# Performance work log

Measured on AMD Instinct MI355X. Metric: run time of the kernel, lower is better.

Reference implementation:

```python
import jax, jax.numpy as jnp
import numpy as np

CLIP_LIMIT = 40.0
TILES = 8  # tileGridSize=(8,8)
BINS = 256


def masked_normalize(x, mask, lo, hi):
    # Faithful to Preprocessor.normalize: if mask nonempty and masked max>0,
    # rescale masked values from [vmin,vmax] -> [lo,hi]; else set masked to lo.
    vmax = jnp.max(jnp.where(mask, x, -jnp.inf))
    vmin = jnp.min(jnp.where(mask, x, jnp.inf))
    cond = jnp.any(mask) & (vmax > 0.0)
    rng = jnp.maximum(vmax - vmin, jnp.float32(1e-12))  # guard degenerate case
    scaled = (x - vmin) / rng * (hi - lo) + lo
    return jnp.where(mask, jnp.where(cond, scaled, jnp.float32(lo)), x)


def clahe_apply(img, clip_limit, T):
    # img: (H, W) int32 in [0, 255]. OpenCV-style CLAHE: per-tile clipped
    # histogram equalization LUTs + bilinear interpolation between tile LUTs.
    H, W = img.shape
    th, tw = H // T, W // T
    area = th * tw
    # per-tile histograms via segment_sum (memory-light, no one-hot blowup)
    ty = jnp.arange(H, dtype=jnp.int32) // th
    tx = jnp.arange(W, dtype=jnp.int32) // tw
    tile_id = ty[:, None] * T + tx[None, :]  # (H, W)
    seg = (tile_id * BINS + img).reshape(-1)
    hist = jax.ops.segment_sum(
        jnp.ones(H * W, jnp.float32), seg, num_segments=T * T * BINS
    ).reshape(T * T, BINS)
    # clip + redistribute excess (uniform batch + stepped residual, OpenCV-style)
    cl = max(int(clip_limit * area / BINS), 1)
    excess = jnp.sum(jnp.maximum(hist - cl, 0.0), axis=1, keepdims=True)
    hist = jnp.minimum(hist, float(cl))
    batch = jnp.floor(excess / BINS)
    residual = excess - batch * BINS  # in [0, 256)
    ar = jnp.arange(BINS, dtype=jnp.float32)
    step = jnp.maximum(jnp.floor(BINS / jnp.maximum(residual, 1.0)), 1.0)
    res_add = ((jnp.mod(ar, step) == 0.0) & (jnp.floor(ar / step) < residual)).astype(jnp.float32)
    hist = hist + batch + res_add
    # LUT from CDF
    cdf = jnp.cumsum(hist, axis=1)
    lut = jnp.clip(jnp.round(cdf * (255.0 / area)), 0.0, 255.0).reshape(T, T, BINS)
    # bilinear interpolation between the 4 surrounding tile LUTs
    fy = (jnp.arange(H, dtype=jnp.float32) + 0.5) / th - 0.5
    fx = (jnp.arange(W, dtype=jnp.float32) + 0.5) / tw - 0.5
    y0 = jnp.clip(jnp.floor(fy).astype(jnp.int32), 0, T - 1)
    x0 = jnp.clip(jnp.floor(fx).astype(jnp.int32), 0, T - 1)
    y1 = jnp.clip(y0 + 1, 0, T - 1)
    x1 = jnp.clip(x0 + 1, 0, T - 1)
    wy = (fy - jnp.floor(fy))[:, None]  # (H,1); at clamped borders both LUTs equal
    wx = (fx - jnp.floor(fx))[None, :]  # (1,W)
    v00 = lut[y0[:, None], x0[None, :], img]
    v01 = lut[y0[:, None], x1[None, :], img]
    v10 = lut[y1[:, None], x0[None, :], img]
    v11 = lut[y1[:, None], x1[None, :], img]
    return (v00 * (1 - wy) * (1 - wx) + v01 * (1 - wy) * wx
            + v10 * wy * (1 - wx) + v11 * wy * wx)


def contrast(x):
    # (X*255).to(uint8) truncates; values in [0,1] so plain floor + clip
    xb = jnp.clip(jnp.floor(x * 255.0), 0.0, 255.0).astype(jnp.int32)
    zero = xb == 0
    nz_cnt = jnp.sum(~zero)
    mean_nz = jnp.floor(
        jnp.sum(jnp.where(zero, 0, xb).astype(jnp.float32)) / jnp.maximum(nz_cnt, 1)
    ).astype(jnp.int32)
    filled = jnp.where(zero & (nz_cnt > 0), mean_nz, xb)
    eq = clahe_apply(filled, CLIP_LIMIT, TILES)
    eq = jnp.where(zero, 0.0, eq)
    return eq / 255.0


def _process_channel(x):  # x: (H, W)
    mask = x > 0.0
    x = masked_normalize(x, mask, 0.0, 1.0)
    x = contrast(x)
    x = masked_normalize(x, mask, 1.0 / 255.0, 1.0)
    return x


def setup_inputs() -> dict:
    key = jax.random.key(0)
    X = jax.random.uniform(key, (1, 4, 4096, 4096), dtype=jnp.float32)
    return {"X": X}


def reference(X):
    # X: (1, C, H, W); channels are processed independently
    out = jax.vmap(_process_channel)(X[0])
    return out[None]
```

## Files before the change

### kernel.cpp

```cpp
#include <hip/hip_runtime.h>
#include <stdint.h>
#include <math.h>

#define NPC 16777216
#define NF4 4194304

struct ChScalars {
  int vmin1, vmax1;
  int vmin2, vmax2;
  int mean_nz, nzpos;
  int pad0, pad1;
};

__device__ __forceinline__ int binof(float x, int cond1, float vmin, float rng) {
  float t = (x > 0.0f) ? (cond1 ? (x - vmin) / rng : 0.0f) : x;
  float b = floorf(t * 255.0f);
  b = fminf(fmaxf(b, 0.0f), 255.0f);
  return (int)b;
}

__global__ __launch_bounds__(256) void k_init(ChScalars* S, unsigned* hist) {
  int g = blockIdx.x * 256 + threadIdx.x;
  hist[g] = 0u;
  if (g < 4) {
    S[g].vmin1 = 0x7FFFFFFF;
    S[g].vmax1 = 0;
    S[g].vmin2 = 0x7FFFFFFF;
    S[g].vmax2 = 0x80000000;
    S[g].mean_nz = 0;
    S[g].nzpos = 0;
    S[g].pad0 = 0; S[g].pad1 = 0;
  }
}

__global__ __launch_bounds__(256) void k_minmax1(const float* __restrict__ X,
                                                 ChScalars* __restrict__ S) {
  const int ch = blockIdx.y;
  const float4* xp = reinterpret_cast<const float4*>(X) + (size_t)ch * NF4;
  const int g = blockIdx.x * 256 + threadIdx.x;
  int mn = 0x7FFFFFFF, mx = 0;
  #pragma unroll
  for (int i = 0; i < 16; ++i) {
    float4 v = xp[(size_t)i * 262144 + g];
    if (v.x > 0.0f) { int b = __float_as_int(v.x); mn = min(mn, b); mx = max(mx, b); }
    if (v.y > 0.0f) { int b = __float_as_int(v.y); mn = min(mn, b); mx = max(mx, b); }
    if (v.z > 0.0f) { int b = __float_as_int(v.z); mn = min(mn, b); mx = max(mx, b); }
    if (v.w > 0.0f) { int b = __float_as_int(v.w); mn = min(mn, b); mx = max(mx, b); }
  }
  __shared__ int smn[256], smx[256];
  smn[threadIdx.x] = mn; smx[threadIdx.x] = mx;
  __syncthreads();
  for (int st = 128; st > 0; st >>= 1) {
    if (threadIdx.x < st) {
      smn[threadIdx.x] = min(smn[threadIdx.x], smn[threadIdx.x + st]);
      smx[threadIdx.x] = max(smx[threadIdx.x], smx[threadIdx.x + st]);
    }
    __syncthreads();
  }
  if (threadIdx.x == 0) {
    atomicMin(&S[ch].vmin1, smn[0]);
    atomicMax(&S[ch].vmax1, smx[0]);
  }
}

__global__ __launch_bounds__(256) void k_hist(const float* __restrict__ X,
                                              const ChScalars* __restrict__ S,
                                              unsigned* __restrict__ hist) {
  const int ch = blockIdx.z;
  __shared__ unsigned lh[256];
  lh[threadIdx.x] = 0u;
  __syncthreads();
  const ChScalars s = S[ch];
  const int cond1 = s.vmax1 > 0;
  const float vmin = __int_as_float(s.vmin1);
  const float rng = fmaxf(__int_as_float(s.vmax1) - vmin, 1e-12f);
  const int X0 = blockIdx.x << 8, Y0 = blockIdx.y << 6;
  const float4* xp = reinterpret_cast<const float4*>(X) + (size_t)ch * NF4;
  for (int i = 0; i < 16; ++i) {
    int fidx = i * 256 + threadIdx.x;
    int r = fidx >> 6, c4 = fidx & 63;
    float4 v = xp[(size_t)(Y0 + r) * 1024 + (X0 >> 2) + c4];
    atomicAdd(&lh[binof(v.x, cond1, vmin, rng)], 1u);
    atomicAdd(&lh[binof(v.y, cond1, vmin, rng)], 1u);
    atomicAdd(&lh[binof(v.z, cond1, vmin, rng)], 1u);
    atomicAdd(&lh[binof(v.w, cond1, vmin, rng)], 1u);
  }
  __syncthreads();
  const int tile = ((Y0 >> 9) << 3) + (X0 >> 9);
  atomicAdd(&hist[((ch << 6) + tile) * 256 + threadIdx.x], lh[threadIdx.x]);
}

__global__ __launch_bounds__(256) void k_stats(const unsigned* __restrict__ hist,
                                               ChScalars* __restrict__ S) {
  const int ch = blockIdx.x, b = threadIdx.x;
  unsigned long long cnt = 0;
  for (int t = 0; t < 64; ++t) cnt += hist[((ch << 6) + t) * 256 + b];
  __shared__ unsigned long long sh[256];
  __shared__ unsigned long long zc;
  if (b == 0) zc = cnt;
  sh[b] = (b == 0) ? 0ULL : (unsigned long long)b * cnt;
  __syncthreads();
  for (int st = 128; st > 0; st >>= 1) {
    if (b < st) sh[b] += sh[b + st];
    __syncthreads();
  }
  if (b == 0) {
    long long nz = 16777216LL - (long long)zc;
    float sumf = (float)sh[0];
    long long d = (nz < 1) ? 1 : nz;
    S[ch].mean_nz = (int)floor((double)sumf / (double)d);
    S[ch].nzpos = (nz > 0) ? 1 : 0;
  }
}

__global__ __launch_bounds__(256) void k_lut(const unsigned* __restrict__ hist,
                                             const ChScalars* __restrict__ S,
                                             float* __restrict__ lut) {
  const int ch = blockIdx.y, tile = blockIdx.x, b = threadIdx.x;
  const ChScalars s = S[ch];
  const unsigned* hrow = hist + ((ch << 6) + tile) * 256;
  float h = (float)hrow[b];
  if (s.nzpos && s.mean_nz != 0) {
    unsigned h0 = hrow[0];
    if (b == 0) h = 0.0f;
    if (b == s.mean_nz) h += (float)h0;
  }
  __shared__ float sh[256];
  sh[b] = fmaxf(h - 40960.0f, 0.0f);
  __syncthreads();
  for (int st = 128; st > 0; st >>= 1) {
    if (b < st) sh[b] += sh[b + st];
    __syncthreads();
  }
  const float excess = sh[0];
  __syncthreads();
  float hc = fminf(h, 40960.0f);
  float batch = floorf(excess / 256.0f);
  float residual = excess - batch * 256.0f;
  float step = fmaxf(floorf(256.0f / fmaxf(residual, 1.0f)), 1.0f);
  float fb = (float)b;
  float res_add = ((fmodf(fb, step) == 0.0f) && (floorf(fb / step) < residual)) ? 1.0f : 0.0f;
  sh[b] = hc + batch + res_add;
  __syncthreads();
  for (int st = 1; st < 256; st <<= 1) {
    float v = (b >= st) ? sh[b - st] : 0.0f;
    __syncthreads();
    sh[b] += v;
    __syncthreads();
  }
  float l = rintf(sh[b] * (255.0f / 262144.0f));
  lut[((ch << 6) + tile) * 256 + b] = fminf(fmaxf(l, 0.0f), 255.0f);
}

template <bool WRITE>
__global__ __launch_bounds__(256) void k_apply(const float* __restrict__ X,
                                               const ChScalars* __restrict__ Sin,
                                               const float* __restrict__ lut,
                                               ChScalars* __restrict__ Smut,
                                               float* __restrict__ out) {
  const int ch = blockIdx.z;
  const int X0 = blockIdx.x << 8, Y0 = blockIdx.y << 6;
  const ChScalars s = Sin[ch];
  const int cond1 = s.vmax1 > 0;
  const float vmin = __int_as_float(s.vmin1);
  const float rng = fmaxf(__int_as_float(s.vmax1) - vmin, 1e-12f);
  const int iy0 = (Y0 < 256) ? -1 : ((Y0 - 256) >> 9);
  const int ix0 = (X0 < 256) ? -1 : ((X0 - 256) >> 9);
  const int y0t = (iy0 < 0) ? 0 : iy0;
  const int y1t = (iy0 + 1 > 7) ? 7 : (iy0 + 1);
  const int x0t = (ix0 < 0) ? 0 : ix0;
  const int x1t = (ix0 + 1 > 7) ? 7 : (ix0 + 1);
  __shared__ float L[4][256];
  const float* lc = lut + (size_t)(ch << 6) * 256;
  L[0][threadIdx.x] = lc[(y0t * 8 + x0t) * 256 + threadIdx.x];
  L[1][threadIdx.x] = lc[(y0t * 8 + x1t) * 256 + threadIdx.x];
  L[2][threadIdx.x] = lc[(y1t * 8 + x0t) * 256 + threadIdx.x];
  L[3][threadIdx.x] = lc[(y1t * 8 + x1t) * 256 + threadIdx.x];
  __syncthreads();
  const int cond2 = (s.vmax1 > 0) && (__int_as_float(s.vmax2) > 0.0f);
  const float vmin2 = __int_as_float(s.vmin2);
  const float rng2 = fmaxf(__int_as_float(s.vmax2) - vmin2, 1e-12f);
  const float LO = (float)(1.0 / 255.0);
  const float SC = (float)(1.0 - 1.0 / 255.0);
  const float4* xp = reinterpret_cast<const float4*>(X) + (size_t)ch * NF4;
  float4* op = WRITE ? (reinterpret_cast<float4*>(out) + (size_t)ch * NF4) : nullptr;
  int mn = 0x7FFFFFFF, mx = 0x80000000;
  for (int i = 0; i < 16; ++i) {
    int fidx = i * 256 + threadIdx.x;
    int r = fidx >> 6, c4 = fidx & 63;
    int y = Y0 + r;
    int xpx = X0 + (c4 << 2);
    size_t f4i = (size_t)y * 1024 + (X0 >> 2) + c4;
    float4 v = xp[f4i];
    float fy = ((float)y + 0.5f) / 512.0f - 0.5f;
    float wy = fy - floorf(fy);
    float vv[4] = {v.x, v.y, v.z, v.w};
    float res[4];
    #pragma unroll
    for (int k = 0; k < 4; ++k) {
      float xv = vv[k];
      float fx = ((float)(xpx + k) + 0.5f) / 512.0f - 0.5f;
      float wx = fx - floorf(fx);
      int xb = binof(xv, cond1, vmin, rng);
      int zero = (xb == 0);
      int f = (zero && s.nzpos) ? s.mean_nz : xb;
      float eq = L[0][f] * (1.0f - wy) * (1.0f - wx)
               + L[1][f] * (1.0f - wy) * wx
               + L[2][f] * wy * (1.0f - wx)
               + L[3][f] * wy * wx;
      if (zero) eq = 0.0f;
      float cval = eq / 255.0f;
      if (WRITE) {
        float o;
        if (xv > 0.0f) o = cond2 ? ((cval - vmin2) / rng2 * SC + LO) : LO;
        else o = cval;
        res[k] = o;
      } else {
        if (xv > 0.0f) {
          int bb = __float_as_int(cval);
          mn = min(mn, bb);
          mx = max(mx, bb);
        }
      }
    }
    if (WRITE) {
      float4 o4 = make_float4(res[0], res[1], res[2], res[3]);
      op[f4i] = o4;
    }
  }
  if (!WRITE) {
    __shared__ int smn[256], smx[256];
    smn[threadIdx.x] = mn; smx[threadIdx.x] = mx;
    __syncthreads();
    for (int st = 128; st > 0; st >>= 1) {
      if (threadIdx.x < st) {
        smn[threadIdx.x] = min(smn[threadIdx.x], smn[threadIdx.x + st]);
        smx[threadIdx.x] = max(smx[threadIdx.x], smx[threadIdx.x + st]);
      }
      __syncthreads();
    }
    if (threadIdx.x == 0) {
      atomicMin(&Smut[ch].vmin2, smn[0]);
      atomicMax(&Smut[ch].vmax2, smx[0]);
    }
  }
}

extern "C" void kernel_launch(void* const* d_in, const int* in_sizes, int n_in,
                              void* d_out, int out_size, void* d_ws, size_t ws_size,
                              hipStream_t stream) {
  const float* X = (const float*)d_in[0];
  float* out = (float*)d_out;
  char* ws = (char*)d_ws;
  ChScalars* S = (ChScalars*)ws;
  unsigned* hist = (unsigned*)(ws + 256);
  float* lut = (float*)(ws + 256 + 65536 * 4);

  k_init<<<256, 256, 0, stream>>>(S, hist);
  k_minmax1<<<dim3(1024, 4, 1), 256, 0, stream>>>(X, S);
  k_hist<<<dim3(16, 64, 4), 256, 0, stream>>>(X, S, hist);
  k_stats<<<4, 256, 0, stream>>>(hist, S);
  k_lut<<<dim3(64, 4, 1), 256, 0, stream>>>(hist, S, lut);
  k_apply<false><<<dim3(16, 64, 4), 256, 0, stream>>>(X, S, lut, S, nullptr);
  k_apply<true><<<dim3(16, 64, 4), 256, 0, stream>>>(X, S, lut, S, out);
}
```

Measured before the change: 690.7 us.

## Reverse block order for L2 reuse, fuse stats into LUT kernel, vectorize LUT reads

Launches k_hist and the write pass of k_apply in reversed block order, so they start on the tail of the input that the previous pass touched last and may still find it in cache. The per-channel stats computation moves into every k_lut block, which removes one launch but repeats the reduction 64 times per channel. The four tile LUTs are packed into one float4 per bin so a single LDS read serves each pixel, and the x weights are hoisted out of the loop. Output stores become nontemporal, and the min/max pass now tracks eq instead of eq/255, dividing by 255 afterwards, which can shift results by float rounding.

```diff
diff --git a/kernel.cpp b/kernel.cpp
--- a/kernel.cpp
+++ b/kernel.cpp
@@ -4,6 +4,8 @@
 
 #define NPC 16777216
 #define NF4 4194304
+
+typedef float f32x4 __attribute__((ext_vector_type(4)));
 
 struct ChScalars {
   int vmin1, vmax1;
@@ -74,7 +76,8 @@
   const int cond1 = s.vmax1 > 0;
   const float vmin = __int_as_float(s.vmin1);
   const float rng = fmaxf(__int_as_float(s.vmax1) - vmin, 1e-12f);
-  const int X0 = blockIdx.x << 8, Y0 = blockIdx.y << 6;
+  const int X0 = (15 - (int)blockIdx.x) << 8;
+  const int Y0 = (63 - (int)blockIdx.y) << 6;
   const float4* xp = reinterpret_cast<const float4*>(X) + (size_t)ch * NF4;
   for (int i = 0; i < 16; ++i) {
     int fidx = i * 256 + threadIdx.x;
@@ -90,40 +93,33 @@
   atomicAdd(&hist[((ch << 6) + tile) * 256 + threadIdx.x], lh[threadIdx.x]);
 }
 
-__global__ __launch_bounds__(256) void k_stats(const unsigned* __restrict__ hist,
-                                               ChScalars* __restrict__ S) {
-  const int ch = blockIdx.x, b = threadIdx.x;
+__global__ __launch_bounds__(256) void k_lut(const unsigned* __restrict__ hist,
+                                             ChScalars* __restrict__ S,
+                                             float* __restrict__ lut) {
+  const int ch = blockIdx.y, tile = blockIdx.x, b = threadIdx.x;
   unsigned long long cnt = 0;
   for (int t = 0; t < 64; ++t) cnt += hist[((ch << 6) + t) * 256 + b];
-  __shared__ unsigned long long sh[256];
-  __shared__ unsigned long long zc;
-  if (b == 0) zc = cnt;
-  sh[b] = (b == 0) ? 0ULL : (unsigned long long)b * cnt;
+  __shared__ unsigned long long sh64[256];
+  __shared__ unsigned zc;
+  if (b == 0) zc = (unsigned)cnt;
+  sh64[b] = (b == 0) ? 0ULL : (unsigned long long)b * cnt;
   __syncthreads();
   for (int st = 128; st > 0; st >>= 1) {
-    if (b < st) sh[b] += sh[b + st];
-    __syncthreads();
-  }
-  if (b == 0) {
-    long long nz = 16777216LL - (long long)zc;
-    float sumf = (float)sh[0];
-    long long d = (nz < 1) ? 1 : nz;
-    S[ch].mean_nz = (int)floor((double)sumf / (double)d);
-    S[ch].nzpos = (nz > 0) ? 1 : 0;
-  }
-}
-
-__global__ __launch_bounds__(256) void k_lut(const unsigned* __restrict__ hist,
-                                             const ChScalars* __restrict__ S,
-                                             float* __restrict__ lut) {
-  const int ch = blockIdx.y, tile = blockIdx.x, b = threadIdx.x;
-  const ChScalars s = S[ch];
+    if (b < st) sh64[b] += sh64[b + st];
+    __syncthreads();
+  }
+  const long long nz = 16777216LL - (long long)zc;
+  const float sumf = (float)sh64[0];
+  const long long d = (nz < 1) ? 1 : nz;
+  const int mean_nz = (int)floor((double)sumf / (double)d);
+  const int nzpos = (nz > 0) ? 1 : 0;
+  if (tile == 0 && b == 0) { S[ch].mean_nz = mean_nz; S[ch].nzpos = nzpos; }
   const unsigned* hrow = hist + ((ch << 6) + tile) * 256;
   float h = (float)hrow[b];
-  if (s.nzpos && s.mean_nz != 0) {
+  if (nzpos && mean_nz != 0) {
     unsigned h0 = hrow[0];
     if (b == 0) h = 0.0f;
-    if (b == s.mean_nz) h += (float)h0;
+    if (b == mean_nz) h += (float)h0;
   }
   __shared__ float sh[256];
   sh[b] = fmaxf(h - 40960.0f, 0.0f);
@@ -159,7 +155,9 @@
                                                ChScalars* __restrict__ Smut,
                                                float* __restrict__ out) {
   const int ch = blockIdx.z;
-  const int X0 = blockIdx.x << 8, Y0 = blockIdx.y << 6;
+  const int bx = WRITE ? (15 - (int)blockIdx.x) : (int)blockIdx.x;
+  const int by = WRITE ? (63 - (int)blockIdx.y) : (int)blockIdx.y;
+  const int X0 = bx << 8, Y0 = by << 6;
   const ChScalars s = Sin[ch];
   const int cond1 = s.vmax1 > 0;
   const float vmin = __int_as_float(s.vmin1);
@@ -170,62 +168,74 @@
   const int y1t = (iy0 + 1 > 7) ? 7 : (iy0 + 1);
   const int x0t = (ix0 < 0) ? 0 : ix0;
   const int x1t = (ix0 + 1 > 7) ? 7 : (ix0 + 1);
-  __shared__ float L[4][256];
-  const float* lc = lut + (size_t)(ch << 6) * 256;
-  L[0][threadIdx.x] = lc[(y0t * 8 + x0t) * 256 + threadIdx.x];
-  L[1][threadIdx.x] = lc[(y0t * 8 + x1t) * 256 + threadIdx.x];
-  L[2][threadIdx.x] = lc[(y1t * 8 + x0t) * 256 + threadIdx.x];
-  L[3][threadIdx.x] = lc[(y1t * 8 + x1t) * 256 + threadIdx.x];
-  __syncthreads();
-  const int cond2 = (s.vmax1 > 0) && (__int_as_float(s.vmax2) > 0.0f);
-  const float vmin2 = __int_as_float(s.vmin2);
-  const float rng2 = fmaxf(__int_as_float(s.vmax2) - vmin2, 1e-12f);
+  __shared__ f32x4 L4[256];
+  {
+    const float* lc = lut + (size_t)(ch << 6) * 256;
+    f32x4 Lv;
+    Lv.x = lc[(y0t * 8 + x0t) * 256 + threadIdx.x];
+    Lv.y = lc[(y0t * 8 + x1t) * 256 + threadIdx.x];
+    Lv.z = lc[(y1t * 8 + x0t) * 256 + threadIdx.x];
+    Lv.w = lc[(y1t * 8 + x1t) * 256 + threadIdx.x];
+    L4[threadIdx.x] = Lv;
+  }
+  __syncthreads();
+  const float vmax2c = __int_as_float(s.vmax2) / 255.0f;
+  const float vmin2c = __int_as_float(s.vmin2) / 255.0f;
+  const int cond2 = (s.vmax1 > 0) && (vmax2c > 0.0f);
+  const float rng2 = fmaxf(vmax2c - vmin2c, 1e-12f);
   const float LO = (float)(1.0 / 255.0);
   const float SC = (float)(1.0 - 1.0 / 255.0);
+  const int c4 = threadIdx.x & 63;
+  const int r0 = threadIdx.x >> 6;
+  float wxk[4], omwxk[4];
+  #pragma unroll
+  for (int k = 0; k < 4; ++k) {
+    float fx = ((float)(X0 + (c4 << 2) + k) + 0.5f) / 512.0f - 0.5f;
+    float w = fx - floorf(fx);
+    wxk[k] = w;
+    omwxk[k] = 1.0f - w;
+  }
   const float4* xp = reinterpret_cast<const float4*>(X) + (size_t)ch * NF4;
-  float4* op = WRITE ? (reinterpret_cast<float4*>(out) + (size_t)ch * NF4) : nullptr;
+  float* op = WRITE ? (out + (size_t)ch * NPC) : nullptr;
   int mn = 0x7FFFFFFF, mx = 0x80000000;
   for (int i = 0; i < 16; ++i) {
-    int fidx = i * 256 + threadIdx.x;
-    int r = fidx >> 6, c4 = fidx & 63;
-    int y = Y0 + r;
-    int xpx = X0 + (c4 << 2);
-    size_t f4i = (size_t)y * 1024 + (X0 >> 2) + c4;
-    float4 v = xp[f4i];
-    float fy = ((float)y + 0.5f) / 512.0f - 0.5f;
-    float wy = fy - floorf(fy);
+    const int y = Y0 + i * 4 + r0;
+    const size_t f4i = (size_t)y * 1024 + (X0 >> 2) + c4;
+    const float4 v = xp[f4i];
+    const float fy = ((float)y + 0.5f) / 512.0f - 0.5f;
+    const float wy = fy - floorf(fy);
+    const float omwy = 1.0f - wy;
     float vv[4] = {v.x, v.y, v.z, v.w};
     float res[4];
     #pragma unroll
     for (int k = 0; k < 4; ++k) {
       float xv = vv[k];
-      float fx = ((float)(xpx + k) + 0.5f) / 512.0f - 0.5f;
-      float wx = fx - floorf(fx);
       int xb = binof(xv, cond1, vmin, rng);
       int zero = (xb == 0);
       int f = (zero && s.nzpos) ? s.mean_nz : xb;
-      float eq = L[0][f] * (1.0f - wy) * (1.0f - wx)
-               + L[1][f] * (1.0f - wy) * wx
-               + L[2][f] * wy * (1.0f - wx)
-               + L[3][f] * wy * wx;
+      f32x4 Lv = L4[f];
+      float eq = Lv.x * omwy * omwxk[k]
+               + Lv.y * omwy * wxk[k]
+               + Lv.z * wy * omwxk[k]
+               + Lv.w * wy * wxk[k];
       if (zero) eq = 0.0f;
-      float cval = eq / 255.0f;
       if (WRITE) {
+        float cval = eq / 255.0f;
         float o;
-        if (xv > 0.0f) o = cond2 ? ((cval - vmin2) / rng2 * SC + LO) : LO;
+        if (xv > 0.0f) o = cond2 ? ((cval - vmin2c) / rng2 * SC + LO) : LO;
         else o = cval;
         res[k] = o;
       } else {
         if (xv > 0.0f) {
-          int bb = __float_as_int(cval);
+          int bb = __float_as_int(eq);
           mn = min(mn, bb);
           mx = max(mx, bb);
         }
       }
     }
     if (WRITE) {
-      float4 o4 = make_float4(res[0], res[1], res[2], res[3]);
-      op[f4i] = o4;
+      f32x4 o4 = {res[0], res[1], res[2], res[3]};
+      __builtin_nontemporal_store(o4, reinterpret_cast<f32x4*>(op) + f4i);
     }
   }
   if (!WRITE) {
@@ -259,7 +269,6 @@
   k_init<<<256, 256, 0, stream>>>(S, hist);
   k_minmax1<<<dim3(1024, 4, 1), 256, 0, stream>>>(X, S);
   k_hist<<<dim3(16, 64, 4), 256, 0, stream>>>(X, S, hist);
-  k_stats<<<4, 256, 0, stream>>>(hist, S);
   k_lut<<<dim3(64, 4, 1), 256, 0, stream>>>(hist, S, lut);
   k_apply<false><<<dim3(16, 64, 4), 256, 0, stream>>>(X, S, lut, S, nullptr);
   k_apply<true><<<dim3(16, 64, 4), 256, 0, stream>>>(X, S, lut, S, out);
```

Result: faster. 668.5 us (-3.2%).
